# Kernel optimization log

Measured on AMD Instinct MI355X. Metric: run time of the kernel, lower is better.

## Reference

```python
import jax, jax.numpy as jnp
import numpy as np

HID = 512
ROLES = 64

def setup_inputs() -> dict:
    key = jax.random.key(0)
    k1, k2, k3, k4, k5 = jax.random.split(key, 5)
    pred_input = jax.random.normal(k1, (8, 512, HID), dtype=jnp.float32)
    args_input = jax.random.normal(k2, (8, 512, HID), dtype=jnp.float32)
    # learned params (orthogonal init approximated by scaled normal for testing)
    U = jax.random.normal(k3, (HID, ROLES, HID), dtype=jnp.float32) * 0.02
    bias1 = jax.random.normal(k4, (1, HID * ROLES), dtype=jnp.float32) * 0.02
    bias2 = jax.random.normal(k5, (1, ROLES), dtype=jnp.float32) * 0.02
    return {"pred_input": pred_input, "args_input": args_input,
            "U": U, "bias1": bias1, "bias2": bias2}

def reference(pred_input, args_input, U, bias1, bias2):
    # dropout p=0.0 -> identity (eval behavior)
    b, t, h = pred_input.shape
    n = b * t
    pred = pred_input.reshape(n, h)          # [n, h]
    args = args_input.reshape(n, h)          # [n, h]
    # first = pred @ U.view(h, R*h) + bias1  -> [n, R*h]
    first = pred @ U.reshape(h, -1) + bias1
    # batched bilinear reduction: [n, R, h] x [n, h] -> [n, R]
    out = jnp.einsum('nrk,nk->nr', first.reshape(n, ROLES, h), args)
    return out + bias2
```

## Files before the change

kernel.cpp:

```cpp
#include <hip/hip_runtime.h>
#include <stdint.h>


#define HID   512
#define ROLES 64
#define NTOK  4096
#define BM    128
#define BN    128
#define BK    64

typedef __attribute__((ext_vector_type(8))) _Float16 f16x8;
typedef __attribute__((ext_vector_type(4))) _Float16 f16x4;
typedef __attribute__((ext_vector_type(4))) float    f32x4;

__device__ __forceinline__ void async16(const void* g, void* l) {
  __builtin_amdgcn_global_load_lds(
      (const __attribute__((address_space(1))) uint32_t*)g,
      (__attribute__((address_space(3))) uint32_t*)l, 16, 0, 0);
}

__global__ __launch_bounds__(256) void cvt_pred(const float* __restrict__ in,
                                                _Float16* __restrict__ outp,
                                                float* __restrict__ o,
                                                const float* __restrict__ b2) {
  const int idx = blockIdx.x * 256 + threadIdx.x;
  const float4 v = ((const float4*)in)[idx];
  f16x4 t;
  t[0] = (_Float16)v.x; t[1] = (_Float16)v.y;
  t[2] = (_Float16)v.z; t[3] = (_Float16)v.w;
  ((f16x4*)outp)[idx] = t;
  if (idx < NTOK * ROLES) o[idx] = b2[idx & (ROLES - 1)];
}

__global__ __launch_bounds__(256) void cvt_u(const float* __restrict__ U,
                                             _Float16* __restrict__ ut) {
  __shared__ float tile[128][129];
  const int h0 = blockIdx.x * 128, k0 = blockIdx.y * 128, r = blockIdx.z;
  const int t = threadIdx.x;
  const int rr = t >> 5, c4 = (t & 31) * 4;
#pragma unroll
  for (int pass = 0; pass < 16; pass++) {
    const int row = pass * 8 + rr;
    const float4 v = *(const float4*)(U + ((size_t)(h0 + row) * ROLES + r) * HID + k0 + c4);
    tile[row][c4 + 0] = v.x; tile[row][c4 + 1] = v.y;
    tile[row][c4 + 2] = v.z; tile[row][c4 + 3] = v.w;
  }
  __syncthreads();
  const int kr = t >> 4, hc = (t & 15) * 8;
#pragma unroll
  for (int pass = 0; pass < 8; pass++) {
    const int k = pass * 16 + kr;
    alignas(16) _Float16 hb[8];
#pragma unroll
    for (int j = 0; j < 8; j++) hb[j] = (_Float16)tile[hc + j][k];
    *(uint4*)(ut + ((size_t)r * HID + k0 + k) * HID + h0 + hc) = *(const uint4*)hb;
  }
}

__global__ __launch_bounds__(256, 3) void bilinear_mfma(
    const _Float16* __restrict__ predf, const _Float16* __restrict__ utf,
    const float* __restrict__ args, const float* __restrict__ bias1,
    float* __restrict__ out) {
  __shared__ _Float16 sA[BM * BK];
  __shared__ _Float16 sB[BN * BK];

  const int nblk = blockIdx.x, mblk = blockIdx.y, r = blockIdx.z;
  const int m0 = mblk * BM, n0 = nblk * BN;
  const int tid  = threadIdx.x;
  const int wave = tid >> 6, lane = tid & 63;
  const int col  = lane & 15, quad = lane >> 4;
  const int wm = (wave & 1) * 64, wn = (wave >> 1) * 64;

  const int i_loc = tid >> 3;
  const int ko    = ((tid & 7) ^ (i_loc & 7)) * 8;
  const size_t offA = (size_t)(m0 + i_loc) * HID + ko;
  const size_t offB = ((size_t)r * HID + n0 + i_loc) * HID + ko;
  const int ldsW = wave * 512;

  const int slotL8 = (quad ^ (col & 7)) * 8;
  const int slotH8 = slotL8 ^ 32;
  int rowA[4], rowB[4];
#pragma unroll
  for (int mt = 0; mt < 4; mt++) rowA[mt] = (wm + mt * 16 + col) * BK;
#pragma unroll
  for (int nt = 0; nt < 4; nt++) rowB[nt] = (wn + nt * 16 + col) * BK;

  f32x4 acc[4][4];
#pragma unroll
  for (int a = 0; a < 4; a++)
#pragma unroll
    for (int b = 0; b < 4; b++) acc[a][b] = (f32x4){0.f, 0.f, 0.f, 0.f};

  for (int k0 = 0; k0 < HID; k0 += BK) {
#pragma unroll
    for (int c = 0; c < 4; c++) {
      async16(predf + offA + (size_t)(c * 32) * HID + k0, sA + c * 2048 + ldsW);
      async16(utf   + offB + (size_t)(c * 32) * HID + k0, sB + c * 2048 + ldsW);
    }
    __syncthreads();

    {
      f16x8 a[4], b[4];
#pragma unroll
      for (int mt = 0; mt < 4; mt++) a[mt] = *(const f16x8*)(sA + rowA[mt] + slotL8);
#pragma unroll
      for (int nt = 0; nt < 4; nt++) b[nt] = *(const f16x8*)(sB + rowB[nt] + slotL8);
#pragma unroll
      for (int mt = 0; mt < 4; mt++)
#pragma unroll
        for (int nt = 0; nt < 4; nt++)
          acc[mt][nt] = __builtin_amdgcn_mfma_f32_16x16x32_f16(a[mt], b[nt], acc[mt][nt], 0, 0, 0);
    }
    {
      f16x8 a[4], b[4];
#pragma unroll
      for (int mt = 0; mt < 4; mt++) a[mt] = *(const f16x8*)(sA + rowA[mt] + slotH8);
#pragma unroll
      for (int nt = 0; nt < 4; nt++) b[nt] = *(const f16x8*)(sB + rowB[nt] + slotH8);
#pragma unroll
      for (int mt = 0; mt < 4; mt++)
#pragma unroll
        for (int nt = 0; nt < 4; nt++)
          acc[mt][nt] = __builtin_amdgcn_mfma_f32_16x16x32_f16(a[mt], b[nt], acc[mt][nt], 0, 0, 0);
    }
    __syncthreads();
  }

  float b1v[4];
#pragma unroll
  for (int nt = 0; nt < 4; nt++)
    b1v[nt] = bias1[r * HID + n0 + wn + nt * 16 + col];

#pragma unroll
  for (int mt = 0; mt < 4; mt++) {
#pragma unroll
    for (int reg = 0; reg < 4; reg++) {
      const int m = m0 + wm + mt * 16 + quad * 4 + reg;
      const float* arow = args + (size_t)m * HID + n0 + wn + col;
      float s = 0.f;
#pragma unroll
      for (int nt = 0; nt < 4; nt++)
        s += (acc[mt][nt][reg] + b1v[nt]) * arow[nt * 16];
      s += __shfl_xor(s, 1);
      s += __shfl_xor(s, 2);
      s += __shfl_xor(s, 4);
      s += __shfl_xor(s, 8);
      if (col == 0) atomicAdd(out + (size_t)m * ROLES + r, s);
    }
  }
}

__global__ __launch_bounds__(256) void fallback_k(
    const float* __restrict__ pred, const float* __restrict__ args,
    const float* __restrict__ U, const float* __restrict__ b1,
    const float* __restrict__ b2, float* __restrict__ out) {
  const int idx = blockIdx.x * 256 + threadIdx.x;
  const int r = idx >> 12;
  const int n = idx & (NTOK - 1);
  const float* arow = args + (size_t)n * HID;
  const float* prow = pred + (size_t)n * HID;
  float acc = 0.f;
  for (int h = 0; h < HID; h++) {
    const float* urow = U + ((size_t)h * ROLES + r) * HID;
    float s = 0.f;
    for (int k = 0; k < HID; k++) s = fmaf(urow[k], arow[k], s);
    acc = fmaf(prow[h], s, acc);
  }
  float sb = 0.f;
  const float* brow = b1 + (size_t)r * HID;
  for (int k = 0; k < HID; k++) sb = fmaf(brow[k], arow[k], sb);
  out[(size_t)n * ROLES + r] = acc + sb + b2[r];
}

extern "C" void kernel_launch(void* const* d_in, const int* in_sizes, int n_in,
                              void* d_out, int out_size, void* d_ws, size_t ws_size,
                              hipStream_t stream) {
  const float* pred = (const float*)d_in[0];
  const float* args = (const float*)d_in[1];
  const float* U    = (const float*)d_in[2];
  const float* b1   = (const float*)d_in[3];
  const float* b2   = (const float*)d_in[4];
  float* out = (float*)d_out;

  const size_t PRED_ELEMS = (size_t)NTOK * HID;
  const size_t U_ELEMS    = (size_t)HID * ROLES * HID;
  const size_t WS_NEEDED  = (PRED_ELEMS + U_ELEMS) * sizeof(_Float16);

  if (ws_size < WS_NEEDED) {
    hipLaunchKernelGGL(fallback_k, dim3((NTOK * ROLES) / 256), dim3(256), 0, stream,
                       pred, args, U, b1, b2, out);
    return;
  }

  _Float16* predf = (_Float16*)d_ws;
  _Float16* utf   = predf + PRED_ELEMS;

  hipLaunchKernelGGL(cvt_pred, dim3((unsigned)(PRED_ELEMS / 4 / 256)), dim3(256), 0, stream,
                     pred, predf, out, b2);
  hipLaunchKernelGGL(cvt_u, dim3(HID / 128, HID / 128, ROLES), dim3(256), 0, stream,
                     U, utf);
  hipLaunchKernelGGL(bilinear_mfma, dim3(HID / BN, NTOK / BM, ROLES), dim3(256), 0, stream,
                     predf, utf, args, b1, out);
}
```

Baseline: 322.3 us.

## Loop over all N tiles per block and replace atomics with direct stores

Each block now iterates over all hidden-dimension column tiles for its token rows and role. It accumulates the bilinear partial sums in registers, reduces across waves via shared memory, and writes the final output with bias2 directly. This removes the global atomicAdd traffic and the separate output initialisation in the conversion kernel. In exchange the grid is four times smaller and each block runs four times longer, which reduces available parallelism and tail balance.

```diff
diff --git a/kernel.cpp b/kernel.cpp
--- a/kernel.cpp
+++ b/kernel.cpp
@@ -20,16 +20,13 @@
 }
 
 __global__ __launch_bounds__(256) void cvt_pred(const float* __restrict__ in,
-                                                _Float16* __restrict__ outp,
-                                                float* __restrict__ o,
-                                                const float* __restrict__ b2) {
+                                                _Float16* __restrict__ outp) {
   const int idx = blockIdx.x * 256 + threadIdx.x;
   const float4 v = ((const float4*)in)[idx];
   f16x4 t;
   t[0] = (_Float16)v.x; t[1] = (_Float16)v.y;
   t[2] = (_Float16)v.z; t[3] = (_Float16)v.w;
   ((f16x4*)outp)[idx] = t;
-  if (idx < NTOK * ROLES) o[idx] = b2[idx & (ROLES - 1)];
 }
 
 __global__ __launch_bounds__(256) void cvt_u(const float* __restrict__ U,
@@ -60,12 +57,12 @@
 __global__ __launch_bounds__(256, 3) void bilinear_mfma(
     const _Float16* __restrict__ predf, const _Float16* __restrict__ utf,
     const float* __restrict__ args, const float* __restrict__ bias1,
-    float* __restrict__ out) {
+    const float* __restrict__ bias2, float* __restrict__ out) {
   __shared__ _Float16 sA[BM * BK];
   __shared__ _Float16 sB[BN * BK];
 
-  const int nblk = blockIdx.x, mblk = blockIdx.y, r = blockIdx.z;
-  const int m0 = mblk * BM, n0 = nblk * BN;
+  const int mblk = blockIdx.x, r = blockIdx.y;
+  const int m0 = mblk * BM;
   const int tid  = threadIdx.x;
   const int wave = tid >> 6, lane = tid & 63;
   const int col  = lane & 15, quad = lane >> 4;
@@ -73,8 +70,8 @@
 
   const int i_loc = tid >> 3;
   const int ko    = ((tid & 7) ^ (i_loc & 7)) * 8;
-  const size_t offA = (size_t)(m0 + i_loc) * HID + ko;
-  const size_t offB = ((size_t)r * HID + n0 + i_loc) * HID + ko;
+  const size_t offA  = (size_t)(m0 + i_loc) * HID + ko;
+  const size_t offB0 = ((size_t)r * HID + i_loc) * HID + ko;
   const int ldsW = wave * 512;
 
   const int slotL8 = (quad ^ (col & 7)) * 8;
@@ -85,68 +82,106 @@
 #pragma unroll
   for (int nt = 0; nt < 4; nt++) rowB[nt] = (wn + nt * 16 + col) * BK;
 
-  f32x4 acc[4][4];
+  float s_part[4][4];
 #pragma unroll
   for (int a = 0; a < 4; a++)
 #pragma unroll
-    for (int b = 0; b < 4; b++) acc[a][b] = (f32x4){0.f, 0.f, 0.f, 0.f};
-
-  for (int k0 = 0; k0 < HID; k0 += BK) {
-#pragma unroll
-    for (int c = 0; c < 4; c++) {
-      async16(predf + offA + (size_t)(c * 32) * HID + k0, sA + c * 2048 + ldsW);
-      async16(utf   + offB + (size_t)(c * 32) * HID + k0, sB + c * 2048 + ldsW);
+    for (int b = 0; b < 4; b++) s_part[a][b] = 0.f;
+
+  for (int n0 = 0; n0 < HID; n0 += BN) {
+    const size_t offB = offB0 + (size_t)n0 * HID;
+
+    f32x4 acc[4][4];
+#pragma unroll
+    for (int a = 0; a < 4; a++)
+#pragma unroll
+      for (int b = 0; b < 4; b++) acc[a][b] = (f32x4){0.f, 0.f, 0.f, 0.f};
+
+    for (int k0 = 0; k0 < HID; k0 += BK) {
+#pragma unroll
+      for (int c = 0; c < 4; c++) {
+        async16(predf + offA + (size_t)(c * 32) * HID + k0, sA + c * 2048 + ldsW);
+        async16(utf   + offB + (size_t)(c * 32) * HID + k0, sB + c * 2048 + ldsW);
+      }
+      __syncthreads();
+
+      {
+        f16x8 a[4], b[4];
+#pragma unroll
+        for (int mt = 0; mt < 4; mt++) a[mt] = *(const f16x8*)(sA + rowA[mt] + slotL8);
+#pragma unroll
+        for (int nt = 0; nt < 4; nt++) b[nt] = *(const f16x8*)(sB + rowB[nt] + slotL8);
+#pragma unroll
+        for (int mt = 0; mt < 4; mt++)
+#pragma unroll
+          for (int nt = 0; nt < 4; nt++)
+            acc[mt][nt] = __builtin_amdgcn_mfma_f32_16x16x32_f16(a[mt], b[nt], acc[mt][nt], 0, 0, 0);
+      }
+      {
+        f16x8 a[4], b[4];
+#pragma unroll
+        for (int mt = 0; mt < 4; mt++) a[mt] = *(const f16x8*)(sA + rowA[mt] + slotH8);
+#pragma unroll
+        for (int nt = 0; nt < 4; nt++) b[nt] = *(const f16x8*)(sB + rowB[nt] + slotH8);
+#pragma unroll
+        for (int mt = 0; mt < 4; mt++)
+#pragma unroll
+          for (int nt = 0; nt < 4; nt++)
+            acc[mt][nt] = __builtin_amdgcn_mfma_f32_16x16x32_f16(a[mt], b[nt], acc[mt][nt], 0, 0, 0);
+      }
+      __syncthreads();
     }
-    __syncthreads();
-
-    {
-      f16x8 a[4], b[4];
-#pragma unroll
-      for (int mt = 0; mt < 4; mt++) a[mt] = *(const f16x8*)(sA + rowA[mt] + slotL8);
-#pragma unroll
-      for (int nt = 0; nt < 4; nt++) b[nt] = *(const f16x8*)(sB + rowB[nt] + slotL8);
-#pragma unroll
-      for (int mt = 0; mt < 4; mt++)
+
+    float b1v[4];
+#pragma unroll
+    for (int nt = 0; nt < 4; nt++)
+      b1v[nt] = bias1[r * HID + n0 + wn + nt * 16 + col];
+
+#pragma unroll
+    for (int mt = 0; mt < 4; mt++) {
+#pragma unroll
+      for (int reg = 0; reg < 4; reg++) {
+        const int m = m0 + wm + mt * 16 + quad * 4 + reg;
+        const float* arow = args + (size_t)m * HID + n0 + wn + col;
+        float s = s_part[mt][reg];
 #pragma unroll
         for (int nt = 0; nt < 4; nt++)
-          acc[mt][nt] = __builtin_amdgcn_mfma_f32_16x16x32_f16(a[mt], b[nt], acc[mt][nt], 0, 0, 0);
+          s += (acc[mt][nt][reg] + b1v[nt]) * arow[nt * 16];
+        s_part[mt][reg] = s;
+      }
     }
-    {
-      f16x8 a[4], b[4];
-#pragma unroll
-      for (int mt = 0; mt < 4; mt++) a[mt] = *(const f16x8*)(sA + rowA[mt] + slotH8);
-#pragma unroll
-      for (int nt = 0; nt < 4; nt++) b[nt] = *(const f16x8*)(sB + rowB[nt] + slotH8);
-#pragma unroll
-      for (int mt = 0; mt < 4; mt++)
-#pragma unroll
-        for (int nt = 0; nt < 4; nt++)
-          acc[mt][nt] = __builtin_amdgcn_mfma_f32_16x16x32_f16(a[mt], b[nt], acc[mt][nt], 0, 0, 0);
-    }
-    __syncthreads();
-  }
-
-  float b1v[4];
-#pragma unroll
-  for (int nt = 0; nt < 4; nt++)
-    b1v[nt] = bias1[r * HID + n0 + wn + nt * 16 + col];
-
-#pragma unroll
-  for (int mt = 0; mt < 4; mt++) {
+  }
+
+#pragma unroll
+  for (int mt = 0; mt < 4; mt++)
 #pragma unroll
     for (int reg = 0; reg < 4; reg++) {
-      const int m = m0 + wm + mt * 16 + quad * 4 + reg;
-      const float* arow = args + (size_t)m * HID + n0 + wn + col;
-      float s = 0.f;
-#pragma unroll
-      for (int nt = 0; nt < 4; nt++)
-        s += (acc[mt][nt][reg] + b1v[nt]) * arow[nt * 16];
+      float s = s_part[mt][reg];
       s += __shfl_xor(s, 1);
       s += __shfl_xor(s, 2);
       s += __shfl_xor(s, 4);
       s += __shfl_xor(s, 8);
-      if (col == 0) atomicAdd(out + (size_t)m * ROLES + r, s);
+      s_part[mt][reg] = s;
     }
+
+  float* red = (float*)sA;
+  if (wave >= 2 && col == 0) {
+#pragma unroll
+    for (int mt = 0; mt < 4; mt++)
+#pragma unroll
+      for (int reg = 0; reg < 4; reg++)
+        red[wm + mt * 16 + quad * 4 + reg] = s_part[mt][reg];
+  }
+  __syncthreads();
+  if (wave < 2 && col == 0) {
+    const float b2v = bias2[r];
+#pragma unroll
+    for (int mt = 0; mt < 4; mt++)
+#pragma unroll
+      for (int reg = 0; reg < 4; reg++) {
+        const int row = wm + mt * 16 + quad * 4 + reg;
+        out[(size_t)(m0 + row) * ROLES + r] = s_part[mt][reg] + red[row] + b2v;
+      }
   }
 }
 
@@ -196,9 +231,9 @@
   _Float16* utf   = predf + PRED_ELEMS;
 
   hipLaunchKernelGGL(cvt_pred, dim3((unsigned)(PRED_ELEMS / 4 / 256)), dim3(256), 0, stream,
-                     pred, predf, out, b2);
+                     pred, predf);
   hipLaunchKernelGGL(cvt_u, dim3(HID / 128, HID / 128, ROLES), dim3(256), 0, stream,
                      U, utf);
-  hipLaunchKernelGGL(bilinear_mfma, dim3(HID / BN, NTOK / BM, ROLES), dim3(256), 0, stream,
-                     predf, utf, args, b1, out);
-}
+  hipLaunchKernelGGL(bilinear_mfma, dim3(NTOK / BM, ROLES), dim3(256), 0, stream,
+                     predf, utf, args, b1, b2, out);
+}
```

After: 352.7 us. 1.09x slower.
